# Performance work log

Measured on AMD Instinct MI355X. Metric: run time of the kernel, lower is better.

## Reference

```python
import jax, jax.numpy as jnp
import numpy as np

E = 1024   # embedding_dim
H = 64     # head_size
B, T = 8, 2048

def setup_inputs() -> dict:
    key = jax.random.key(0)
    k1, k2, k3, k4 = jax.random.split(key, 4)
    s = 1.0 / np.sqrt(E)
    return {
        "x": jax.random.normal(k1, (B, T, E), dtype=jnp.float32),
        "Wq": jax.random.normal(k2, (E, H), dtype=jnp.float32) * s,
        "Wk": jax.random.normal(k3, (E, H), dtype=jnp.float32) * s,
        "Wv": jax.random.normal(k4, (E, H), dtype=jnp.float32) * s,
    }

def reference(x, Wq, Wk, Wv):
    # projections: [B,T,E] @ [E,H] -> [B,T,H]
    q = x @ Wq
    k = x @ Wk
    v = x @ Wv
    Tq = x.shape[1]
    # scaled scores [B,T,T], masked causal softmax, then @ V
    wei = jnp.einsum('bth,bsh->bts', q, k) * (H ** -0.5)
    causal = jnp.tril(jnp.ones((Tq, Tq), dtype=bool))
    wei = jnp.where(causal, wei, -jnp.inf)
    attn = jax.nn.softmax(wei, axis=-1)
    return attn @ v
```

## Files before the change

### kernel.cpp

```cpp
#include <hip/hip_runtime.h>

#define E  1024
#define H  64
#define BB 8
#define TT 2048

typedef __attribute__((ext_vector_type(8)))  short bf16x8;
typedef __attribute__((ext_vector_type(4)))  float f32x4;
typedef __attribute__((ext_vector_type(16))) float f32x16;
typedef __attribute__((ext_vector_type(8)))  short short8;
typedef __attribute__((ext_vector_type(4)))  short short4v;
typedef __attribute__((ext_vector_type(4)))  unsigned u32x4;

__device__ __forceinline__ short f2bf(float f) {
    union { float f; unsigned u; } v; v.f = f;
    unsigned r = v.u + 0x7FFFu + ((v.u >> 16) & 1u);
    return (short)(r >> 16);
}

__device__ __forceinline__ float fexp2(float x) {
    float r;
    asm("v_exp_f32 %0, %1" : "=v"(r) : "v"(x));
    return r;
}

__device__ __forceinline__ bf16x8 asbf(u32x4 v) {
    bf16x8 r;
    __builtin_memcpy(&r, &v, 16);
    return r;
}

__device__ __forceinline__ bf16x8 cvt8u(u32x4 a, u32x4 b) {
    unsigned w0, w1, w2, w3;
    float a0 = __uint_as_float(a[0]), a1 = __uint_as_float(a[1]);
    float a2 = __uint_as_float(a[2]), a3 = __uint_as_float(a[3]);
    float b0 = __uint_as_float(b[0]), b1 = __uint_as_float(b[1]);
    float b2 = __uint_as_float(b[2]), b3 = __uint_as_float(b[3]);
    asm("v_cvt_pk_bf16_f32 %0, %1, %2" : "=v"(w0) : "v"(a0), "v"(a1));
    asm("v_cvt_pk_bf16_f32 %0, %1, %2" : "=v"(w1) : "v"(a2), "v"(a3));
    asm("v_cvt_pk_bf16_f32 %0, %1, %2" : "=v"(w2) : "v"(b0), "v"(b1));
    asm("v_cvt_pk_bf16_f32 %0, %1, %2" : "=v"(w3) : "v"(b2), "v"(b3));
    u32x4 u = {w0, w1, w2, w3};
    return asbf(u);
}

#define GLD(dst, p) \
    asm volatile("global_load_dwordx4 %0, %1, off" \
                 : "=v"(dst) : "v"((unsigned long long)(p)) : "memory")

__global__ __launch_bounds__(256)
void pack_w3(const float* __restrict__ Wq, const float* __restrict__ Wk,
             const float* __restrict__ Wv, short* __restrict__ Wb3)
{
    const int t  = blockIdx.x * 256 + threadIdx.x;
    const int l  = t & 63;
    const int f  = (t >> 6) % 12;
    const int sc = t / 768;
    const int n  = f * 16 + (l & 15);
    const int m  = n >> 6, nn = n & 63;
    const float* W = (m == 0) ? Wq : (m == 1 ? Wk : Wv);
    const int k0 = sc * 32 + ((l >> 4) << 3);
    short8 o;
    #pragma unroll
    for (int j = 0; j < 8; ++j) o[j] = f2bf(W[(k0 + j) * 64 + nn]);
    *(short8*)&Wb3[(size_t)t * 8] = o;
}

__global__ __attribute__((amdgpu_waves_per_eu(1, 2))) __launch_bounds__(256)
void proj_v13(const float* __restrict__ x, const short* __restrict__ Wb3,
              short* __restrict__ q, short* __restrict__ k, short* __restrict__ vt)
{
    const int t  = threadIdx.x;
    const int l  = t & 63;
    const int w  = t >> 6;
    const int rg = w & 1, cg = w >> 1;
    const int l15 = l & 15, g = l >> 4;
    const long row0 = (long)blockIdx.x * 64;

    f32x4 acc[2][6] = {};

    const float* ax0 = x + (row0 + rg * 32 + l15) * E + g * 8;
    const float* ax1 = x + (row0 + rg * 32 + 16 + l15) * E + g * 8;
    const short* bp = Wb3 + ((size_t)(cg * 6) * 64 + l) * 8;

    u32x4 xA0, xA1, xA2, xA3, yA0, yA1, yA2, yA3, yA4, yA5;
    u32x4 xB0, xB1, xB2, xB3, yB0, yB1, yB2, yB3, yB4, yB5;

#define ISSUE_A(s) do { \
    GLD(xA0, ax0 + (s) * 32); GLD(xA1, ax0 + (s) * 32 + 4); \
    GLD(xA2, ax1 + (s) * 32); GLD(xA3, ax1 + (s) * 32 + 4); \
    GLD(yA0, bp + ((size_t)(s) * 12 + 0) * 512); \
    GLD(yA1, bp + ((size_t)(s) * 12 + 1) * 512); \
    GLD(yA2, bp + ((size_t)(s) * 12 + 2) * 512); \
    GLD(yA3, bp + ((size_t)(s) * 12 + 3) * 512); \
    GLD(yA4, bp + ((size_t)(s) * 12 + 4) * 512); \
    GLD(yA5, bp + ((size_t)(s) * 12 + 5) * 512); \
} while (0)
#define ISSUE_B(s) do { \
    GLD(xB0, ax0 + (s) * 32); GLD(xB1, ax0 + (s) * 32 + 4); \
    GLD(xB2, ax1 + (s) * 32); GLD(xB3, ax1 + (s) * 32 + 4); \
    GLD(yB0, bp + ((size_t)(s) * 12 + 0) * 512); \
    GLD(yB1, bp + ((size_t)(s) * 12 + 1) * 512); \
    GLD(yB2, bp + ((size_t)(s) * 12 + 2) * 512); \
    GLD(yB3, bp + ((size_t)(s) * 12 + 3) * 512); \
    GLD(yB4, bp + ((size_t)(s) * 12 + 4) * 512); \
    GLD(yB5, bp + ((size_t)(s) * 12 + 5) * 512); \
} while (0)
#define COMPUTE(X0, X1, X2, X3, Y0, Y1, Y2, Y3, Y4, Y5) do { \
    bf16x8 af0 = cvt8u(X0, X1); \
    bf16x8 af1 = cvt8u(X2, X3); \
    acc[0][0] = __builtin_amdgcn_mfma_f32_16x16x32_bf16(af0, asbf(Y0), acc[0][0], 0, 0, 0); \
    acc[1][0] = __builtin_amdgcn_mfma_f32_16x16x32_bf16(af1, asbf(Y0), acc[1][0], 0, 0, 0); \
    acc[0][1] = __builtin_amdgcn_mfma_f32_16x16x32_bf16(af0, asbf(Y1), acc[0][1], 0, 0, 0); \
    acc[1][1] = __builtin_amdgcn_mfma_f32_16x16x32_bf16(af1, asbf(Y1), acc[1][1], 0, 0, 0); \
    acc[0][2] = __builtin_amdgcn_mfma_f32_16x16x32_bf16(af0, asbf(Y2), acc[0][2], 0, 0, 0); \
    acc[1][2] = __builtin_amdgcn_mfma_f32_16x16x32_bf16(af1, asbf(Y2), acc[1][2], 0, 0, 0); \
    acc[0][3] = __builtin_amdgcn_mfma_f32_16x16x32_bf16(af0, asbf(Y3), acc[0][3], 0, 0, 0); \
    acc[1][3] = __builtin_amdgcn_mfma_f32_16x16x32_bf16(af1, asbf(Y3), acc[1][3], 0, 0, 0); \
    acc[0][4] = __builtin_amdgcn_mfma_f32_16x16x32_bf16(af0, asbf(Y4), acc[0][4], 0, 0, 0); \
    acc[1][4] = __builtin_amdgcn_mfma_f32_16x16x32_bf16(af1, asbf(Y4), acc[1][4], 0, 0, 0); \
    acc[0][5] = __builtin_amdgcn_mfma_f32_16x16x32_bf16(af0, asbf(Y5), acc[0][5], 0, 0, 0); \
    acc[1][5] = __builtin_amdgcn_mfma_f32_16x16x32_bf16(af1, asbf(Y5), acc[1][5], 0, 0, 0); \
} while (0)

    ISSUE_A(0);
    for (int s2 = 0; s2 < 16; ++s2) {
        const int s = 2 * s2;
        ISSUE_B(s + 1);
        asm volatile("s_waitcnt vmcnt(10)" ::: "memory");
        __builtin_amdgcn_sched_barrier(0);
        COMPUTE(xA0, xA1, xA2, xA3, yA0, yA1, yA2, yA3, yA4, yA5);
        if (s2 < 15) {
            ISSUE_A(s + 2);
            asm volatile("s_waitcnt vmcnt(10)" ::: "memory");
        } else {
            asm volatile("s_waitcnt vmcnt(0)" ::: "memory");
        }
        __builtin_amdgcn_sched_barrier(0);
        COMPUTE(xB0, xB1, xB2, xB3, yB0, yB1, yB2, yB3, yB4, yB5);
    }

    #pragma unroll
    for (int rt = 0; rt < 2; ++rt) {
        const long trow = row0 + rg * 32 + rt * 16 + g * 4;
        const long bb   = trow >> 11;
        const int  t0   = (int)(trow & 2047);
        #pragma unroll
        for (int fi = 0; fi < 6; ++fi) {
            const int n = cg * 96 + fi * 16 + l15;
            const int m = n >> 6;
            const int h = n & 63;
            if (m == 2) {
                short4v pkt;
                #pragma unroll
                for (int r = 0; r < 4; ++r) pkt[r] = f2bf(acc[rt][fi][r]);
                *(short4v*)&vt[(bb * 64 + h) * TT + t0] = pkt;
            } else {
                short* base = (m == 0) ? q : k;
                const float sc = (m == 0) ? (0.125f * 1.44269504f) : 1.0f;
                #pragma unroll
                for (int r = 0; r < 4; ++r)
                    base[(trow + r) * 64 + h] = f2bf(acc[rt][fi][r] * sc);
            }
        }
    }
#undef ISSUE_A
#undef ISSUE_B
#undef COMPUTE
}

__global__ __launch_bounds__(512)
void attn_v8(const short* __restrict__ qg,
             const short* __restrict__ kg,
             const short* __restrict__ vtg,
             float* __restrict__ out)
{
    __shared__ float Op[8][32][66];
    __shared__ float Ml[8][32][2];

    const int t   = threadIdx.x;
    const int L   = t & 63;
    const int w   = t >> 6;
    const int bid = blockIdx.x;
    const int b   = bid & 7;
    const int pr  = bid >> 3;
    const int l31 = L & 31, hi = L >> 5;

    const int stA = pr, stB = 63 - pr;
    const int nA = stA + 1;
    int WA = (8 * nA + 32) / 65;
    WA = WA < 1 ? 1 : (WA > 7 ? 7 : WA);
    const int WB = 8 - WA;

    const bool isB  = (w >= WA);
    const int  st   = isB ? stB : stA;
    const int  q0   = st * 32;
    const int  strd = isB ? WB : WA;
    const int  c0   = isB ? (w - WA) : w;

    bf16x8 qf[4];
    {
        const short* qp = qg + ((long)b * TT + q0 + l31) * 64 + hi * 8;
        qf[0] = *(const bf16x8*)(qp);
        qf[1] = *(const bf16x8*)(qp + 16);
        qf[2] = *(const bf16x8*)(qp + 32);
        qf[3] = *(const bf16x8*)(qp + 48);
    }

    f32x16 o0 = {}, o1 = {};
    float mrun = -1e30f, lrun = 0.f;

    const short* kbase = kg  + ((long)b * TT + l31) * 64 + hi * 8;
    const short* vbase = vtg + ((long)b * 64 + l31) * TT + hi * 8;

    for (int ci = c0; ci <= st; ci += strd) {
        const int kvs = ci * 32;
        const short* kp = kbase + (long)kvs * 64;
        bf16x8 kf0 = *(const bf16x8*)(kp);
        bf16x8 kf1 = *(const bf16x8*)(kp + 16);
        bf16x8 kf2 = *(const bf16x8*)(kp + 32);
        bf16x8 kf3 = *(const bf16x8*)(kp + 48);
        const short* vp = vbase + kvs;
        bf16x8 vf00 = *(const bf16x8*)(vp);
        bf16x8 vf01 = *(const bf16x8*)(vp + 16);
        bf16x8 vf10 = *(const bf16x8*)(vp + 32 * TT);
        bf16x8 vf11 = *(const bf16x8*)(vp + 32 * TT + 16);

        f32x16 s = {};
        __builtin_amdgcn_s_setprio(1);
        s = __builtin_amdgcn_mfma_f32_32x32x16_bf16(kf0, qf[0], s, 0, 0, 0);
        s = __builtin_amdgcn_mfma_f32_32x32x16_bf16(kf1, qf[1], s, 0, 0, 0);
        s = __builtin_amdgcn_mfma_f32_32x32x16_bf16(kf2, qf[2], s, 0, 0, 0);
        s = __builtin_amdgcn_mfma_f32_32x32x16_bf16(kf3, qf[3], s, 0, 0, 0);
        __builtin_amdgcn_s_setprio(0);

        if (kvs == q0) {
            #pragma unroll
            for (int r = 0; r < 16; ++r) {
                const int crow = (r & 3) + 8 * (r >> 2) + 4 * hi;
                if (crow > l31) s[r] = -1e30f;
            }
        }
        float m01 = fmaxf(s[0], s[1]),   m23 = fmaxf(s[2], s[3]);
        float m45 = fmaxf(s[4], s[5]),   m67 = fmaxf(s[6], s[7]);
        float m89 = fmaxf(s[8], s[9]),   mab = fmaxf(s[10], s[11]);
        float mcd = fmaxf(s[12], s[13]), mef = fmaxf(s[14], s[15]);
        float mloc = fmaxf(fmaxf(fmaxf(m01, m23), fmaxf(m45, m67)),
                           fmaxf(fmaxf(m89, mab), fmaxf(mcd, mef)));
        mloc = fmaxf(mloc, __shfl_xor(mloc, 32));
        if (__any(mloc > mrun + 8.f)) {
            const float mnew = fmaxf(mrun, mloc);
            const float a = fexp2(mrun - mnew);
            mrun = mnew;
            lrun *= a;
            #pragma unroll
            for (int r = 0; r < 16; ++r) { o0[r] *= a; o1[r] *= a; }
        }
        #pragma unroll
        for (int r = 0; r < 16; ++r) s[r] = fexp2(s[r] - mrun);
        {
            float s01 = (s[0] + s[1]) + (s[2] + s[3]);
            float s23 = (s[4] + s[5]) + (s[6] + s[7]);
            float s45 = (s[8] + s[9]) + (s[10] + s[11]);
            float s67 = (s[12] + s[13]) + (s[14] + s[15]);
            float lsum = (s01 + s23) + (s45 + s67);
            lsum += __shfl_xor(lsum, 32);
            lrun += lsum;
        }
        unsigned wv[8];
        #pragma unroll
        for (int i = 0; i < 8; ++i)
            asm("v_cvt_pk_bf16_f32 %0, %1, %2" : "=v"(wv[i]) : "v"(s[2 * i]), "v"(s[2 * i + 1]));
        unsigned p00 = wv[0], p02 = wv[2];
        unsigned p01 = wv[1], p03 = wv[3];
        unsigned p10 = wv[4], p12 = wv[6];
        unsigned p11 = wv[5], p13 = wv[7];
        asm("v_permlane32_swap_b32 %0, %1" : "+v"(p00), "+v"(p02));
        asm("v_permlane32_swap_b32 %0, %1" : "+v"(p01), "+v"(p03));
        asm("v_permlane32_swap_b32 %0, %1" : "+v"(p10), "+v"(p12));
        asm("v_permlane32_swap_b32 %0, %1" : "+v"(p11), "+v"(p13));
        u32x4 pb0u = {p00, p01, p02, p03};
        u32x4 pb1u = {p10, p11, p12, p13};
        bf16x8 pb0, pb1;
        __builtin_memcpy(&pb0, &pb0u, 16);
        __builtin_memcpy(&pb1, &pb1u, 16);
        __builtin_amdgcn_s_setprio(1);
        o0 = __builtin_amdgcn_mfma_f32_32x32x16_bf16(vf00, pb0, o0, 0, 0, 0);
        o0 = __builtin_amdgcn_mfma_f32_32x32x16_bf16(vf01, pb1, o0, 0, 0, 0);
        o1 = __builtin_amdgcn_mfma_f32_32x32x16_bf16(vf10, pb0, o1, 0, 0, 0);
        o1 = __builtin_amdgcn_mfma_f32_32x32x16_bf16(vf11, pb1, o1, 0, 0, 0);
        __builtin_amdgcn_s_setprio(0);
    }

    #pragma unroll
    for (int r = 0; r < 16; ++r) {
        const int h = (r & 3) + 8 * (r >> 2) + 4 * hi;
        Op[w][l31][h]      = o0[r];
        Op[w][l31][32 + h] = o1[r];
    }
    if (hi == 0) {
        Ml[w][l31][0] = mrun;
        Ml[w][l31][1] = lrun;
    }
    __syncthreads();

    {
        const bool tb   = (w >= 4);
        const int  base = tb ? WA : 0;
        const int  cnt  = tb ? WB : WA;
        const long oq0  = (long)(tb ? stB : stA) * 32;
        #pragma unroll
        for (int rr = 0; rr < 8; ++rr) {
            const int row = (w & 3) * 8 + rr;
            float M = -1e30f;
            for (int j = 0; j < cnt; ++j)
                M = fmaxf(M, Ml[base + j][row][0]);
            float Ls = 0.f, val = 0.f;
            for (int j = 0; j < cnt; ++j) {
                const float a = fexp2(Ml[base + j][row][0] - M);
                Ls  += a * Ml[base + j][row][1];
                val += a * Op[base + j][row][L];
            }
            out[((long)b * TT + oq0 + row) * 64 + L] = val / Ls;
        }
    }
}

extern "C" void kernel_launch(void* const* d_in, const int* in_sizes, int n_in,
                              void* d_out, int out_size, void* d_ws, size_t ws_size,
                              hipStream_t stream)
{
    const float* x  = (const float*)d_in[0];
    const float* Wq = (const float*)d_in[1];
    const float* Wk = (const float*)d_in[2];
    const float* Wv = (const float*)d_in[3];
    float* out = (float*)d_out;

    const size_t n = (size_t)BB * TT * H;
    short* q   = (short*)d_ws;
    short* k   = q + n;
    short* vt  = k + n;
    short* Wb3 = vt + n;

    pack_w3  <<<dim3(96),  256, 0, stream>>>(Wq, Wk, Wv, Wb3);
    proj_v13 <<<dim3(256), 256, 0, stream>>>(x, Wb3, q, k, vt);
    attn_v8  <<<dim3(256), 512, 0, stream>>>(q, k, vt, out);
}
```

Before: 57.81 us.

## Shrink projection tile to 16 rows per block and launch 4x more blocks

The projection kernel now has each block handle 16 rows instead of 64. Each of its 4 waves computes 48 output columns over the same 16 rows, where previously each wave covered 2 row groups by 96 columns. The grid grows from 256 to 1024 blocks, so the 256-CU GPU gets more waves and more memory-level parallelism for streaming x, and per-thread register use drops. The cost is that the packed weights are now reloaded 4 times more often across blocks, and each x row is loaded by all four waves rather than two.

After: 75.95 us. +31.4%, slower.

```diff
diff --git a/kernel.cpp b/kernel.cpp
--- a/kernel.cpp
+++ b/kernel.cpp
@@ -66,107 +66,86 @@
     *(short8*)&Wb3[(size_t)t * 8] = o;
 }
 
-__global__ __attribute__((amdgpu_waves_per_eu(1, 2))) __launch_bounds__(256)
-void proj_v13(const float* __restrict__ x, const short* __restrict__ Wb3,
+__global__ __launch_bounds__(256)
+void proj_v14(const float* __restrict__ x, const short* __restrict__ Wb3,
               short* __restrict__ q, short* __restrict__ k, short* __restrict__ vt)
 {
     const int t  = threadIdx.x;
     const int l  = t & 63;
-    const int w  = t >> 6;
-    const int rg = w & 1, cg = w >> 1;
+    const int cg = t >> 6;
     const int l15 = l & 15, g = l >> 4;
-    const long row0 = (long)blockIdx.x * 64;
-
-    f32x4 acc[2][6] = {};
-
-    const float* ax0 = x + (row0 + rg * 32 + l15) * E + g * 8;
-    const float* ax1 = x + (row0 + rg * 32 + 16 + l15) * E + g * 8;
-    const short* bp = Wb3 + ((size_t)(cg * 6) * 64 + l) * 8;
-
-    u32x4 xA0, xA1, xA2, xA3, yA0, yA1, yA2, yA3, yA4, yA5;
-    u32x4 xB0, xB1, xB2, xB3, yB0, yB1, yB2, yB3, yB4, yB5;
+    const long row0 = (long)blockIdx.x * 16;
+
+    f32x4 acc0 = {0,0,0,0}, acc1 = {0,0,0,0}, acc2 = {0,0,0,0};
+
+    const float* ax = x + (row0 + l15) * E + g * 8;
+    const short* bp = Wb3 + ((size_t)(cg * 3) * 64 + l) * 8;
+
+    u32x4 xA0, xA1, yA0, yA1, yA2;
+    u32x4 xB0, xB1, yB0, yB1, yB2;
 
 #define ISSUE_A(s) do { \
-    GLD(xA0, ax0 + (s) * 32); GLD(xA1, ax0 + (s) * 32 + 4); \
-    GLD(xA2, ax1 + (s) * 32); GLD(xA3, ax1 + (s) * 32 + 4); \
+    GLD(xA0, ax + (s) * 32); GLD(xA1, ax + (s) * 32 + 4); \
     GLD(yA0, bp + ((size_t)(s) * 12 + 0) * 512); \
     GLD(yA1, bp + ((size_t)(s) * 12 + 1) * 512); \
     GLD(yA2, bp + ((size_t)(s) * 12 + 2) * 512); \
-    GLD(yA3, bp + ((size_t)(s) * 12 + 3) * 512); \
-    GLD(yA4, bp + ((size_t)(s) * 12 + 4) * 512); \
-    GLD(yA5, bp + ((size_t)(s) * 12 + 5) * 512); \
 } while (0)
 #define ISSUE_B(s) do { \
-    GLD(xB0, ax0 + (s) * 32); GLD(xB1, ax0 + (s) * 32 + 4); \
-    GLD(xB2, ax1 + (s) * 32); GLD(xB3, ax1 + (s) * 32 + 4); \
+    GLD(xB0, ax + (s) * 32); GLD(xB1, ax + (s) * 32 + 4); \
     GLD(yB0, bp + ((size_t)(s) * 12 + 0) * 512); \
     GLD(yB1, bp + ((size_t)(s) * 12 + 1) * 512); \
     GLD(yB2, bp + ((size_t)(s) * 12 + 2) * 512); \
-    GLD(yB3, bp + ((size_t)(s) * 12 + 3) * 512); \
-    GLD(yB4, bp + ((size_t)(s) * 12 + 4) * 512); \
-    GLD(yB5, bp + ((size_t)(s) * 12 + 5) * 512); \
 } while (0)
-#define COMPUTE(X0, X1, X2, X3, Y0, Y1, Y2, Y3, Y4, Y5) do { \
-    bf16x8 af0 = cvt8u(X0, X1); \
-    bf16x8 af1 = cvt8u(X2, X3); \
-    acc[0][0] = __builtin_amdgcn_mfma_f32_16x16x32_bf16(af0, asbf(Y0), acc[0][0], 0, 0, 0); \
-    acc[1][0] = __builtin_amdgcn_mfma_f32_16x16x32_bf16(af1, asbf(Y0), acc[1][0], 0, 0, 0); \
-    acc[0][1] = __builtin_amdgcn_mfma_f32_16x16x32_bf16(af0, asbf(Y1), acc[0][1], 0, 0, 0); \
-    acc[1][1] = __builtin_amdgcn_mfma_f32_16x16x32_bf16(af1, asbf(Y1), acc[1][1], 0, 0, 0); \
-    acc[0][2] = __builtin_amdgcn_mfma_f32_16x16x32_bf16(af0, asbf(Y2), acc[0][2], 0, 0, 0); \
-    acc[1][2] = __builtin_amdgcn_mfma_f32_16x16x32_bf16(af1, asbf(Y2), acc[1][2], 0, 0, 0); \
-    acc[0][3] = __builtin_amdgcn_mfma_f32_16x16x32_bf16(af0, asbf(Y3), acc[0][3], 0, 0, 0); \
-    acc[1][3] = __builtin_amdgcn_mfma_f32_16x16x32_bf16(af1, asbf(Y3), acc[1][3], 0, 0, 0); \
-    acc[0][4] = __builtin_amdgcn_mfma_f32_16x16x32_bf16(af0, asbf(Y4), acc[0][4], 0, 0, 0); \
-    acc[1][4] = __builtin_amdgcn_mfma_f32_16x16x32_bf16(af1, asbf(Y4), acc[1][4], 0, 0, 0); \
-    acc[0][5] = __builtin_amdgcn_mfma_f32_16x16x32_bf16(af0, asbf(Y5), acc[0][5], 0, 0, 0); \
-    acc[1][5] = __builtin_amdgcn_mfma_f32_16x16x32_bf16(af1, asbf(Y5), acc[1][5], 0, 0, 0); \
+#define COMPUTE(X0, X1, Y0, Y1, Y2) do { \
+    bf16x8 af = cvt8u(X0, X1); \
+    acc0 = __builtin_amdgcn_mfma_f32_16x16x32_bf16(af, asbf(Y0), acc0, 0, 0, 0); \
+    acc1 = __builtin_amdgcn_mfma_f32_16x16x32_bf16(af, asbf(Y1), acc1, 0, 0, 0); \
+    acc2 = __builtin_amdgcn_mfma_f32_16x16x32_bf16(af, asbf(Y2), acc2, 0, 0, 0); \
 } while (0)
 
     ISSUE_A(0);
+    #pragma unroll 4
     for (int s2 = 0; s2 < 16; ++s2) {
         const int s = 2 * s2;
         ISSUE_B(s + 1);
-        asm volatile("s_waitcnt vmcnt(10)" ::: "memory");
+        asm volatile("s_waitcnt vmcnt(5)" ::: "memory");
         __builtin_amdgcn_sched_barrier(0);
-        COMPUTE(xA0, xA1, xA2, xA3, yA0, yA1, yA2, yA3, yA4, yA5);
+        COMPUTE(xA0, xA1, yA0, yA1, yA2);
         if (s2 < 15) {
             ISSUE_A(s + 2);
-            asm volatile("s_waitcnt vmcnt(10)" ::: "memory");
+            asm volatile("s_waitcnt vmcnt(5)" ::: "memory");
         } else {
             asm volatile("s_waitcnt vmcnt(0)" ::: "memory");
         }
         __builtin_amdgcn_sched_barrier(0);
-        COMPUTE(xB0, xB1, xB2, xB3, yB0, yB1, yB2, yB3, yB4, yB5);
-    }
-
-    #pragma unroll
-    for (int rt = 0; rt < 2; ++rt) {
-        const long trow = row0 + rg * 32 + rt * 16 + g * 4;
-        const long bb   = trow >> 11;
-        const int  t0   = (int)(trow & 2047);
-        #pragma unroll
-        for (int fi = 0; fi < 6; ++fi) {
-            const int n = cg * 96 + fi * 16 + l15;
-            const int m = n >> 6;
-            const int h = n & 63;
-            if (m == 2) {
-                short4v pkt;
-                #pragma unroll
-                for (int r = 0; r < 4; ++r) pkt[r] = f2bf(acc[rt][fi][r]);
-                *(short4v*)&vt[(bb * 64 + h) * TT + t0] = pkt;
-            } else {
-                short* base = (m == 0) ? q : k;
-                const float sc = (m == 0) ? (0.125f * 1.44269504f) : 1.0f;
-                #pragma unroll
-                for (int r = 0; r < 4; ++r)
-                    base[(trow + r) * 64 + h] = f2bf(acc[rt][fi][r] * sc);
-            }
-        }
+        COMPUTE(xB0, xB1, yB0, yB1, yB2);
     }
 #undef ISSUE_A
 #undef ISSUE_B
 #undef COMPUTE
+
+    const long trow = row0 + g * 4;
+    const long bb   = trow >> 11;
+    const int  t0   = (int)(trow & 2047);
+    #pragma unroll
+    for (int ni = 0; ni < 3; ++ni) {
+        const f32x4 acc = (ni == 0) ? acc0 : (ni == 1) ? acc1 : acc2;
+        const int n = cg * 48 + ni * 16 + l15;
+        const int m = n >> 6;
+        const int h = n & 63;
+        if (m == 2) {
+            short4v pkt;
+            #pragma unroll
+            for (int r = 0; r < 4; ++r) pkt[r] = f2bf(acc[r]);
+            *(short4v*)&vt[(bb * 64 + h) * TT + t0] = pkt;
+        } else {
+            short* base = (m == 0) ? q : k;
+            const float sc = (m == 0) ? (0.125f * 1.44269504f) : 1.0f;
+            #pragma unroll
+            for (int r = 0; r < 4; ++r)
+                base[(trow + r) * 64 + h] = f2bf(acc[r] * sc);
+        }
+    }
 }
 
 __global__ __launch_bounds__(512)
@@ -342,7 +321,7 @@
     short* vt  = k + n;
     short* Wb3 = vt + n;
 
-    pack_w3  <<<dim3(96),  256, 0, stream>>>(Wq, Wk, Wv, Wb3);
-    proj_v13 <<<dim3(256), 256, 0, stream>>>(x, Wb3, q, k, vt);
-    attn_v8  <<<dim3(256), 512, 0, stream>>>(q, k, vt, out);
-}
+    pack_w3  <<<dim3(96),   256, 0, stream>>>(Wq, Wk, Wv, Wb3);
+    proj_v14 <<<dim3(1024), 256, 0, stream>>>(x, Wb3, q, k, vt);
+    attn_v8  <<<dim3(256),  512, 0, stream>>>(q, k, vt, out);
+}
```
